# Performance work log

Measured on AMD Instinct MI355X. Metric: run time of the kernel, lower is better.

## Reference

```python
import jax, jax.numpy as jnp
import numpy as np

B, S, H, L, V, T = 128, 512, 512, 2, 30, 64  # batch, enc len, hidden, layers, vocab, decode len


def _p(k, shape):
    return jax.random.normal(k, shape, jnp.float32) * 0.05


def setup_inputs() -> dict:
    key = jax.random.key(0)
    ks = jax.random.split(key, 24)
    inp = {"x": jax.random.normal(ks[0], (B, S, 2), jnp.float32)}
    inp["emb"] = _p(ks[1], (V, H))
    # encoder GRU (input dim 2 for layer 0, H for layer 1); PyTorch gate order r,z,n
    inp["enc_Wih0"] = _p(ks[2], (3 * H, 2));  inp["enc_Whh0"] = _p(ks[3], (3 * H, H))
    inp["enc_bih0"] = _p(ks[4], (3 * H,));    inp["enc_bhh0"] = _p(ks[5], (3 * H,))
    inp["enc_Wih1"] = _p(ks[6], (3 * H, H));  inp["enc_Whh1"] = _p(ks[7], (3 * H, H))
    inp["enc_bih1"] = _p(ks[8], (3 * H,));    inp["enc_bhh1"] = _p(ks[9], (3 * H,))
    # decoder GRU (input dim H)
    inp["dec_Wih0"] = _p(ks[10], (3 * H, H)); inp["dec_Whh0"] = _p(ks[11], (3 * H, H))
    inp["dec_bih0"] = _p(ks[12], (3 * H,));   inp["dec_bhh0"] = _p(ks[13], (3 * H,))
    inp["dec_Wih1"] = _p(ks[14], (3 * H, H)); inp["dec_Whh1"] = _p(ks[15], (3 * H, H))
    inp["dec_bih1"] = _p(ks[16], (3 * H,));   inp["dec_bhh1"] = _p(ks[17], (3 * H,))
    inp["fc_W"] = _p(ks[18], (V, 2 * H));     inp["fc_b"] = _p(ks[19], (V,))
    return inp


def gru_cell(xt, h, Wih, Whh, bih, bhh):
    gi = xt @ Wih.T + bih
    gh = h @ Whh.T + bhh
    i_r, i_z, i_n = jnp.split(gi, 3, axis=-1)
    h_r, h_z, h_n = jnp.split(gh, 3, axis=-1)
    r = jax.nn.sigmoid(i_r + h_r)
    z = jax.nn.sigmoid(i_z + h_z)
    n = jnp.tanh(i_n + r * h_n)
    return (1.0 - z) * n + z * h


def _forward(x, emb,
             enc_Wih0, enc_Whh0, enc_bih0, enc_bhh0,
             enc_Wih1, enc_Whh1, enc_bih1, enc_bhh1,
             dec_Wih0, dec_Whh0, dec_bih0, dec_bhh0,
             dec_Wih1, dec_Whh1, dec_bih1, dec_bhh1,
             fc_W, fc_b):
    b = x.shape[0]
    h0 = jnp.zeros((b, H), x.dtype)

    # ---- encoder: 2-layer GRU scanned over time ----
    def enc_step(hs, xt):
        a = gru_cell(xt, hs[0], enc_Wih0, enc_Whh0, enc_bih0, enc_bhh0)
        c = gru_cell(a, hs[1], enc_Wih1, enc_Whh1, enc_bih1, enc_bhh1)
        return (a, c), c

    (e0, e1), out_enc_t = jax.lax.scan(enc_step, (h0, h0), x.transpose(1, 0, 2))
    out_enc = out_enc_t.transpose(1, 0, 2)  # [B, S, H]

    def dec_step(carry, _):
        (d0, d1), tok = carry
        e = emb[tok]  # [B, H]
        n0 = gru_cell(e, d0, dec_Wih0, dec_Whh0, dec_bih0, dec_bhh0)
        n1 = gru_cell(n0, d1, dec_Wih1, dec_Whh1, dec_bih1, dec_bhh1)
        out_dec = n1  # [B, H]
        sim = jnp.einsum('bsh,bh->bs', out_enc, out_dec)  # [B, S]
        # faithful to nn.Softmax() implicit dim on 3-D [B,S,1] tensor -> dim=0 (batch)
        att_w = jax.nn.softmax(sim, axis=0)
        attention = jnp.einsum('bs,bsh->bh', att_w, out_enc)  # [B, H]
        logits = jnp.concatenate([out_dec, attention], axis=-1) @ fc_W.T + fc_b  # [B, V]
        tok_next = jnp.argmax(logits, axis=-1)
        return ((n0, n1), tok_next), logits

    tok0 = jnp.zeros((b,), jnp.int32)
    ((f0, f1), _), logits_t = jax.lax.scan(dec_step, ((e0, e1), tok0), None, length=T)
    vec_out = logits_t.transpose(1, 0, 2)  # [B, T, V]
    hidden = jnp.stack([f0, f1], axis=0)   # [n_layers, B, H]
    return vec_out, hidden


def reference(x, emb,
              enc_Wih0, enc_Whh0, enc_bih0, enc_bhh0,
              enc_Wih1, enc_Whh1, enc_bih1, enc_bhh1,
              dec_Wih0, dec_Whh0, dec_bih0, dec_bhh0,
              dec_Wih1, dec_Whh1, dec_bih1, dec_bhh1,
              fc_W, fc_b):
    return _forward(x, emb,
                    enc_Wih0, enc_Whh0, enc_bih0, enc_bhh0,
                    enc_Wih1, enc_Whh1, enc_bih1, enc_bhh1,
                    dec_Wih0, dec_Whh0, dec_bih0, dec_bhh0,
                    dec_Wih1, dec_Whh1, dec_bih1, dec_bhh1,
                    fc_W, fc_b)
```

## Files before the change

### kernel.cpp

```cpp
#include <hip/hip_runtime.h>
#include <math.h>

typedef short  s16x8 __attribute__((ext_vector_type(8)));
typedef float  f32x4 __attribute__((ext_vector_type(4)));
typedef unsigned short u16;
typedef unsigned long long u64;

#define MFMA16(a, b, c) __builtin_amdgcn_mfma_f32_16x16x32_bf16((a), (b), (c), 0, 0, 0)

#define BB 128
#define SS 512
#define HH 512
#define VV 30
#define TT 64

#define SC_SYS  __HIP_MEMORY_SCOPE_SYSTEM

__device__ __forceinline__ float b2f(u16 v) {
  union { unsigned int u; float f; } c; c.u = ((unsigned int)v) << 16; return c.f;
}
__device__ __forceinline__ u16 f2b(float f) {
  union { float f; unsigned int u; } c; c.f = f;
  unsigned int r = (c.u + 0x7FFFu + ((c.u >> 16) & 1u)) >> 16;
  return (u16)r;
}
__device__ __forceinline__ float sigm(float x) { return 1.f / (1.f + expf(-x)); }
__device__ __forceinline__ s16x8 ldf(const u16* p) { return *(const s16x8*)p; }

__device__ __forceinline__ u64  ld64c(const u64* p)      { return __hip_atomic_load(p, __ATOMIC_RELAXED, SC_SYS); }
__device__ __forceinline__ void st64c(u64* p, u64 v)     { __hip_atomic_store(p, v, __ATOMIC_RELAXED, SC_SYS); }
__device__ __forceinline__ void stf32c(float* p, float v){ __hip_atomic_store(p, v, __ATOMIC_RELAXED, SC_SYS); }
__device__ __forceinline__ float ldf32c(const float* p)  { return __hip_atomic_load(p, __ATOMIC_RELAXED, SC_SYS); }
__device__ __forceinline__ void sti32c(int* p, int v)    { __hip_atomic_store(p, v, __ATOMIC_RELAXED, SC_SYS); }
__device__ __forceinline__ int  ldi32c(const int* p)     { return __hip_atomic_load(p, __ATOMIC_RELAXED, SC_SYS); }
__device__ __forceinline__ void stf32(float* p, float v) { *p = v; }

__device__ unsigned int g_cnt[128];
__device__ float g_smx[SS], g_ssum[SS];

#define C_L0 0
#define C_L1 1
#define C_G0 2
#define C_G1 3
#define C_SIM 4
#define C_SMX 5
#define C_ATT 6

__device__ __forceinline__ void waitp(int idx, int target) {
  if (target <= 0) return;
  unsigned long long t0 = __builtin_amdgcn_s_memrealtime();
  while ((int)__hip_atomic_load(&g_cnt[idx * 16], __ATOMIC_RELAXED, SC_SYS) < target) {
    __builtin_amdgcn_s_sleep(1);
    if (__builtin_amdgcn_s_memrealtime() - t0 > (1ull << 21)) break;
  }
}
__device__ __forceinline__ void waitc2(int i1, int t1, int i2, int t2) {
  if (threadIdx.x == 0) { waitp(i1, t1); waitp(i2, t2); }
  __syncthreads();
}
__device__ __forceinline__ void waitc3(int i1, int t1, int i2, int t2, int i3, int t3) {
  if (threadIdx.x == 0) { waitp(i1, t1); waitp(i2, t2); waitp(i3, t3); }
  __syncthreads();
}
__device__ __forceinline__ void waitc4(int i1, int t1, int i2, int t2, int i3, int t3, int i4, int t4) {
  if (threadIdx.x == 0) { waitp(i1, t1); waitp(i2, t2); waitp(i3, t3); waitp(i4, t4); }
  __syncthreads();
}
__device__ __forceinline__ void arrive(int idx) {
  __syncthreads();
  if (threadIdx.x == 0) {
    asm volatile("s_waitcnt vmcnt(0) lgkmcnt(0)" ::: "memory");
    __hip_atomic_fetch_add(&g_cnt[idx * 16], 1u, __ATOMIC_RELAXED, SC_SYS);
  }
}

__device__ __forceinline__ s16x8 ldl(const u16* buf, int row, int slot) {
  return *(const s16x8*)&buf[(row << 8) + ((slot ^ (row & 15)) << 3)];
}

__device__ __forceinline__ void stage64(u16* SMb, const u16* SRC, int mbase, int kc) {
  const int t = threadIdx.x;
  const u64* base = (const u64*)SRC;
  u64 v[16];
#pragma unroll
  for (int j = 0; j < 16; ++j) {
    const int g = kc * 8 + (j >> 1);
    const int half = j & 1;
    v[j] = ld64c(base + (size_t)(g * 128 + mbase + half * 32) * 8 + t);
  }
#pragma unroll
  for (int j = 0; j < 16; ++j) {
    const int gl = j >> 1, half = j & 1;
    const int row = half * 32 + (t >> 3);
    const int w = t & 7;
    const int s = ((w & 4) << 2) + 2 * gl + ((w >> 1) & 1);
    *(u64*)&SMb[(row << 8) + ((s ^ (row & 15)) << 3) + ((w & 1) << 2)] = v[j];
  }
}

__device__ __forceinline__ void stage128(u16* SM, const u16* SRC, int kc) {
  const int t = threadIdx.x;
  const u64* base = (const u64*)SRC;
  u64 v[32];
#pragma unroll
  for (int j = 0; j < 32; ++j) {
    const int g = kc * 8 + (j >> 2);
    const int q = j & 3;
    v[j] = ld64c(base + (size_t)(g * 128 + q * 32) * 8 + t);
  }
#pragma unroll
  for (int j = 0; j < 32; ++j) {
    const int gl = j >> 2, q = j & 3;
    const int row = q * 32 + (t >> 3);
    const int w = t & 7;
    const int s = ((w & 4) << 2) + 2 * gl + ((w >> 1) & 1);
    *(u64*)&SM[(row << 8) + ((s ^ (row & 15)) << 3) + ((w & 1) << 2)] = v[j];
  }
}


template <bool GATHER, bool COH_H>
__device__ __forceinline__ void gru_dual_staged(
    int bx, u16* SM,
    const u16* __restrict__ A1s, const int* __restrict__ gather,
    const u16* __restrict__ A2s,
    const u16* __restrict__ Wihs, const u16* __restrict__ Whhs,
    const float* __restrict__ bih, const float* __restrict__ bhh,
    float* __restrict__ hf, u16* __restrict__ hs_new,
    u16* __restrict__ oe, size_t oe_mstride)
{
  const int tid  = threadIdx.x;
  const int wave = tid >> 6, lane = tid & 63;
  const int lrow = lane & 15, lq = lane >> 4;
  const int gidx = bx >> 1;
  const int j0 = gidx * 16;
  const int mbase = (bx & 1) * 64;
  const int lr = wave * 16 + lrow;
  const int m0 = mbase + wave * 16;

  const u16* a1p = nullptr;
  if (GATHER)
    a1p = A1s + (size_t)ldi32c(&gather[m0 + lrow]) * 1024 + lq * 8;

  const u16* bp[6];
#pragma unroll
  for (int t = 0; t < 6; ++t) {
    int g = (t < 3) ? t : t - 3;
    const u16* W = (t < 3) ? Wihs : Whhs;
    bp[t] = W + (size_t)(g * HH + j0 + lrow) * 1024 + lq * 8;
  }

  f32x4 acc[6];
#pragma unroll
  for (int t = 0; t < 6; ++t) acc[t] = (f32x4){0.f, 0.f, 0.f, 0.f};

  for (int kc = 0; kc < 4; ++kc) {
    if (!GATHER) stage64(SM, A1s, mbase, kc);
    stage64(SM + 64 * 256, A2s, mbase, kc);
    __syncthreads();
#pragma unroll
    for (int ki = 0; ki < 4; ++ki) {
      const int sl = ki * 4 + lq;
      s16x8 a1h, a1l;
      if (GATHER) { a1h = ldf(a1p); a1l = ldf(a1p + 512); a1p += 32; }
      else        { a1h = ldl(SM, lr, sl); a1l = ldl(SM, lr, 16 + sl); }
      s16x8 a2h = ldl(SM, 64 + lr, sl), a2l = ldl(SM, 64 + lr, 16 + sl);
#pragma unroll
      for (int t = 0; t < 6; ++t) {
        s16x8 bh = ldf(bp[t]), bl = ldf(bp[t] + 512); bp[t] += 32;
        s16x8 ah = (t < 3) ? a1h : a2h;
        s16x8 al = (t < 3) ? a1l : a2l;
        acc[t] = MFMA16(ah, bh, acc[t]);
        acc[t] = MFMA16(ah, bl, acc[t]);
        acc[t] = MFMA16(al, bh, acc[t]);
      }
    }
    __syncthreads();
  }

  const int c = j0 + lrow;
  const float bir = bih[c], biz = bih[HH + c], bin = bih[2 * HH + c];
  const float bhr = bhh[c], bhz = bhh[HH + c], bhn = bhh[2 * HH + c];
  float hvv[4];
#pragma unroll
  for (int r = 0; r < 4; ++r) {
    int m = mbase + wave * 16 + lq * 4 + r;
    float ir = acc[0][r] + bir, iz = acc[1][r] + biz, inn = acc[2][r] + bin;
    float hr = acc[3][r] + bhr, hz = acc[4][r] + bhz, hn = acc[5][r] + bhn;
    float rr = sigm(ir + hr);
    float zz = sigm(iz + hz);
    float nn = tanhf(inn + rr * hn);
    float hp = COH_H ? ldf32c(&hf[(size_t)m * HH + c]) : hf[(size_t)m * HH + c];
    float hv = (1.f - zz) * nn + zz * hp;
    if (COH_H) stf32c(&hf[(size_t)m * HH + c], hv);
    else       stf32(&hf[(size_t)m * HH + c], hv);
    hvv[r] = hv;
    if (oe) oe[(size_t)m * oe_mstride + c] = f2b(hv);
  }
  __syncthreads();
#pragma unroll
  for (int r = 0; r < 4; ++r) {
    const int ml = wave * 16 + lq * 4 + r;
    u16 hi = f2b(hvv[r]);
    SM[ml * 32 + lrow]      = hi;
    SM[ml * 32 + 16 + lrow] = f2b(hvv[r] - b2f(hi));
  }
  __syncthreads();
  {
    u64* dst = (u64*)hs_new + (size_t)(gidx * 128 + mbase) * 8;
    const u64* src = (const u64*)SM;
    st64c(dst + tid,       src[tid]);
    st64c(dst + 256 + tid, src[256 + tid]);
  }
}

__device__ __forceinline__ void gru_l0_staged(
    int bx, int p, u16* SM,
    const float* __restrict__ x, const float* __restrict__ Wih0,
    const u16* __restrict__ Whh0s,
    const float* __restrict__ bih0, const float* __restrict__ bhh0,
    const u16* __restrict__ As,
    float* __restrict__ af, u16* __restrict__ as_new)
{
  const int tid  = threadIdx.x;
  const int wave = tid >> 6, lane = tid & 63;
  const int lrow = lane & 15, lq = lane >> 4;
  const int j0 = bx * 16;
  const int mw = wave * 32;
  const int r0 = mw + lrow, r1 = mw + 16 + lrow;

  const u16* bp[3];
#pragma unroll
  for (int t = 0; t < 3; ++t)
    bp[t] = Whh0s + (size_t)(t * HH + j0 + lrow) * 1024 + lq * 8;

  f32x4 acc[2][3];
#pragma unroll
  for (int i = 0; i < 2; ++i)
#pragma unroll
    for (int t = 0; t < 3; ++t) acc[i][t] = (f32x4){0.f, 0.f, 0.f, 0.f};

  for (int kc = 0; kc < 4; ++kc) {
    stage128(SM, As, kc);
    __syncthreads();
#pragma unroll
    for (int ki = 0; ki < 4; ++ki) {
      const int sl = ki * 4 + lq;
      s16x8 a0h = ldl(SM, r0, sl), a0l = ldl(SM, r0, 16 + sl);
      s16x8 a1h = ldl(SM, r1, sl), a1l = ldl(SM, r1, 16 + sl);
#pragma unroll
      for (int t = 0; t < 3; ++t) {
        s16x8 bh = ldf(bp[t]), bl = ldf(bp[t] + 512); bp[t] += 32;
        acc[0][t] = MFMA16(a0h, bh, acc[0][t]);
        acc[0][t] = MFMA16(a0h, bl, acc[0][t]);
        acc[0][t] = MFMA16(a0l, bh, acc[0][t]);
        acc[1][t] = MFMA16(a1h, bh, acc[1][t]);
        acc[1][t] = MFMA16(a1h, bl, acc[1][t]);
        acc[1][t] = MFMA16(a1l, bh, acc[1][t]);
      }
    }
    __syncthreads();
  }

  const int c = j0 + lrow;
  const float bir = bih0[c], biz = bih0[HH + c], bin = bih0[2 * HH + c];
  const float bhr = bhh0[c], bhz = bhh0[HH + c], bhn = bhh0[2 * HH + c];
  const float wr0 = Wih0[(size_t)c * 2],            wr1 = Wih0[(size_t)c * 2 + 1];
  const float wz0 = Wih0[(size_t)(HH + c) * 2],     wz1 = Wih0[(size_t)(HH + c) * 2 + 1];
  const float wn0 = Wih0[(size_t)(2 * HH + c) * 2], wn1 = Wih0[(size_t)(2 * HH + c) * 2 + 1];
  float hvv[2][4];
#pragma unroll
  for (int tm = 0; tm < 2; ++tm) {
#pragma unroll
    for (int r = 0; r < 4; ++r) {
      int m = mw + tm * 16 + lq * 4 + r;
      float x0 = x[((size_t)m * SS + p) * 2];
      float x1 = x[((size_t)m * SS + p) * 2 + 1];
      float ir  = bir + x0 * wr0 + x1 * wr1;
      float iz  = biz + x0 * wz0 + x1 * wz1;
      float inn = bin + x0 * wn0 + x1 * wn1;
      float hr = acc[tm][0][r] + bhr, hz = acc[tm][1][r] + bhz, hn = acc[tm][2][r] + bhn;
      float rr = sigm(ir + hr);
      float zz = sigm(iz + hz);
      float nn = tanhf(inn + rr * hn);
      float hp = af[(size_t)m * HH + c];
      float hv = (1.f - zz) * nn + zz * hp;
      af[(size_t)m * HH + c] = hv;
      hvv[tm][r] = hv;
    }
  }
  __syncthreads();
#pragma unroll
  for (int tm = 0; tm < 2; ++tm) {
#pragma unroll
    for (int r = 0; r < 4; ++r) {
      const int ml = mw + tm * 16 + lq * 4 + r;
      u16 hi = f2b(hvv[tm][r]);
      SM[ml * 32 + lrow]      = hi;
      SM[ml * 32 + 16 + lrow] = f2b(hvv[tm][r] - b2f(hi));
    }
  }
  __syncthreads();
  {
    u64* dst = (u64*)as_new + (size_t)(bx * 128) * 8;
    const u64* src = (const u64*)SM;
#pragma unroll
    for (int k = 0; k < 4; ++k)
      st64c(dst + k * 256 + tid, src[k * 256 + tid]);
  }
}

__device__ __forceinline__ void sim_block(
    int bx, const float* __restrict__ n1f, const u16* __restrict__ oe,
    float* __restrict__ simt)
{
  const int b = bx >> 1, sc = bx & 1;
  const int wave = threadIdx.x >> 6, lane = threadIdx.x & 63;
  float xr[8];
  const u64* xp = (const u64*)(n1f + (size_t)b * HH + lane * 8);
#pragma unroll
  for (int j = 0; j < 4; ++j) {
    union { u64 q; float f[2]; } u; u.q = ld64c(xp + j);
    xr[2 * j] = u.f[0]; xr[2 * j + 1] = u.f[1];
  }
  int s0 = sc * 256 + wave * 64;
  for (int i = 0; i < 64; ++i) {
    int s = s0 + i;
    s16x8 ov = *(const s16x8*)(oe + ((size_t)b * SS + s) * HH + lane * 8);
    float acc = 0.f;
#pragma unroll
    for (int j = 0; j < 8; ++j) acc += xr[j] * b2f((u16)ov[j]);
    for (int off = 32; off; off >>= 1) acc += __shfl_down(acc, off);
    if (lane == 0) stf32c(&simt[(size_t)s * BB + b], acc);
  }
}

__device__ __forceinline__ void smax_block(int bx, const float* __restrict__ simt)
{
  const int wave = threadIdx.x >> 6, lane = threadIdx.x & 63;
  const int s = bx * 4 + wave;
  union { u64 q; float f[2]; } u;
  u.q = ld64c((const u64*)&simt[(size_t)s * BB + lane * 2]);
  float mx = fmaxf(u.f[0], u.f[1]);
  for (int off = 32; off; off >>= 1) mx = fmaxf(mx, __shfl_xor(mx, off));
  float e = expf(u.f[0] - mx) + expf(u.f[1] - mx);
  for (int off = 32; off; off >>= 1) e += __shfl_xor(e, off);
  if (lane == 0) { stf32c(&g_smx[s], mx); stf32c(&g_ssum[s], e); }
}

__device__ __forceinline__ void attn_block(
    int b, int tstep, const float* __restrict__ simt, const float* __restrict__ n1f,
    const u16* __restrict__ oe, const float* __restrict__ fcW,
    const float* __restrict__ fcb, float* __restrict__ dout,
    int* __restrict__ tok)
{
  __shared__ float wsm[SS];
  __shared__ float xv[2 * HH];
  __shared__ float lg[32];
  const int t = threadIdx.x;

  for (int s = t; s < SS; s += 256) {
    float sv = ldf32c(&simt[(size_t)s * BB + b]);
    float mx = ldf32c(&g_smx[s]);
    float sm = ldf32c(&g_ssum[s]);
    wsm[s] = expf(sv - mx) / sm;
  }
  xv[t]       = ldf32c(&n1f[(size_t)b * HH + t]);
  xv[t + 256] = ldf32c(&n1f[(size_t)b * HH + t + 256]);
  __syncthreads();

  {
    float a0 = 0.f, a1 = 0.f;
    const u16* base = oe + (size_t)b * SS * HH;
    for (int s = 0; s < SS; ++s) {
      float w = wsm[s];
      a0 += w * b2f(base[(size_t)s * HH + t]);
      a1 += w * b2f(base[(size_t)s * HH + t + 256]);
    }
    xv[HH + t]       = a0;
    xv[HH + t + 256] = a1;
  }
  __syncthreads();

  int wave = t >> 6, lane = t & 63;
  for (int v = wave; v < VV; v += 4) {
    const float* wr = fcW + (size_t)v * (2 * HH);
    float acc = 0.f;
#pragma unroll
    for (int i = 0; i < 16; ++i) acc += xv[i * 64 + lane] * wr[i * 64 + lane];
    for (int off = 32; off; off >>= 1) acc += __shfl_down(acc, off);
    if (lane == 0) {
      float lv = acc + fcb[v];
      lg[v] = lv;
      dout[(size_t)b * (TT * VV) + (size_t)tstep * VV + v] = lv;
    }
  }
  __syncthreads();

  if (t == 0) {
    float best = lg[0]; int bi = 0;
    for (int v = 1; v < VV; ++v) if (lg[v] > best) { best = lg[v]; bi = v; }
    sti32c(&tok[b], bi);
  }
}

__global__ __launch_bounds__(256) void enc_persist(
    const float* __restrict__ x, const float* __restrict__ Wih0,
    const u16* __restrict__ Whh0s,
    const float* __restrict__ bih0, const float* __restrict__ bhh0,
    const u16* __restrict__ Wih1s, const u16* __restrict__ Whh1s,
    const float* __restrict__ bih1, const float* __restrict__ bhh1,
    u16* ABF0, u16* ABF1, float* af,
    u16* CBF0, u16* CBF1, float* cf,
    u16* out_enc)
{
  __shared__ u16 SM[32768];
  const int bx = blockIdx.x;
  const u16* pa = ABF0; u16* pa_n = ABF1;
  const u16* pc = CBF0; u16* pc_n = CBF1;
  for (int p = 0; p <= SS; ++p) {
    waitc2(C_L0, 32 * p, C_L1, 64 * (p - 1));
    if (bx < 32) {
      if (p < SS) {
        gru_l0_staged(bx, p, SM, x, Wih0, Whh0s, bih0, bhh0, pa, af, pa_n);
        arrive(C_L0);
      }
    } else {
      if (p > 0) {
        u16* oe = out_enc + (size_t)(p - 1) * HH;
        gru_dual_staged<false, false>(bx - 32, SM, pa, nullptr, pc,
                                      Wih1s, Whh1s, bih1, bhh1,
                                      cf, pc_n, oe, (size_t)SS * HH);
        arrive(C_L1);
      }
    }
    const u16* tp;
    tp = pa; pa = pa_n; pa_n = (u16*)tp;
    tp = pc; pc = pc_n; pc_n = (u16*)tp;
  }
}

__global__ __launch_bounds__(256) void dec_persist(
    const u16* __restrict__ EMBs, int* tok,
    const u16* __restrict__ WdIH0, const u16* __restrict__ WdHH0,
    const float* __restrict__ dbih0, const float* __restrict__ dbhh0,
    const u16* __restrict__ WdIH1, const u16* __restrict__ WdHH1,
    const float* __restrict__ dbih1, const float* __restrict__ dbhh1,
    float* af, float* cf,
    u16* D0A, u16* D0B, u16* D1A, u16* D1B,
    const u16* __restrict__ oe, float* simt,
    const float* __restrict__ fcW, const float* __restrict__ fcb,
    float* dout)
{
  __shared__ u16 SM[32768];
  const int bx = blockIdx.x;
  const u16* d0c = D0A; u16* d0n = D0B;
  const u16* d1c = D1A; u16* d1n = D1B;
  for (int t = 0; t < TT; ++t) {
    if (bx < 64) {
      waitc3(C_G0, 64 * t, C_ATT, 128 * t, C_G1, 64 * (t - 1));
      gru_dual_staged<true, false>(bx, SM, EMBs, tok, d0c,
                                   WdIH0, WdHH0, dbih0, dbhh0, af, d0n,
                                   nullptr, 0);
      arrive(C_G0);
    }
    { const u16* tp = d0c; d0c = d0n; d0n = (u16*)tp; }

    if (bx < 64) {
      waitc4(C_G0, 64 * (t + 1), C_G1, 64 * t, C_SIM, 256 * t, C_ATT, 128 * t);
      gru_dual_staged<false, true>(bx, SM, d0c, nullptr, d1c,
                                   WdIH1, WdHH1, dbih1, dbhh1, cf, d1n,
                                   nullptr, 0);
      arrive(C_G1);
    }
    { const u16* tp = d1c; d1c = d1n; d1n = (u16*)tp; }

    waitc3(C_G1, 64 * (t + 1), C_SMX, 128 * t, C_ATT, 128 * t);
    sim_block(bx, cf, oe, simt);
    arrive(C_SIM);

    if (bx < 128) {
      waitc2(C_SIM, 256 * (t + 1), C_ATT, 128 * t);
      smax_block(bx, simt);
      arrive(C_SMX);
    }

    if (bx < BB) {
      waitc4(C_SMX, 128 * (t + 1), C_SIM, 256 * (t + 1),
             C_G1, 64 * (t + 1), C_G0, 64 * (t + 1));
      attn_block(bx, t, simt, cf, oe, fcW, fcb, dout, tok);
      arrive(C_ATT);
    }
  }
}

__global__ __launch_bounds__(256) void splitall(
    const float* __restrict__ s0, u16* d0, const float* __restrict__ s1, u16* d1,
    const float* __restrict__ s2, u16* d2, const float* __restrict__ s3, u16* d3,
    const float* __restrict__ s4, u16* d4, const float* __restrict__ s5, u16* d5,
    const float* __restrict__ s6, u16* d6, const float* __restrict__ s7, u16* d7)
{
  const int WN = 3 * HH * HH;
  int i = blockIdx.x * 256 + threadIdx.x;
  const float* s; u16* d; int j;
  if      (i < 1 * WN) { s = s0; d = d0; j = i; }
  else if (i < 2 * WN) { s = s1; d = d1; j = i - 1 * WN; }
  else if (i < 3 * WN) { s = s2; d = d2; j = i - 2 * WN; }
  else if (i < 4 * WN) { s = s3; d = d3; j = i - 3 * WN; }
  else if (i < 5 * WN) { s = s4; d = d4; j = i - 4 * WN; }
  else if (i < 6 * WN) { s = s5; d = d5; j = i - 5 * WN; }
  else if (i < 7 * WN) { s = s6; d = d6; j = i - 6 * WN; }
  else { j = i - 7 * WN; if (j >= VV * HH) return; s = s7; d = d7; }
  int r = j >> 9, k = j & 511;
  float v = s[j];
  u16 hi = f2b(v);
  d[(size_t)r * 1024 + k]       = hi;
  d[(size_t)r * 1024 + 512 + k] = f2b(v - b2f(hi));
}

__global__ __launch_bounds__(256) void initk(
    float* af, float* cf, u16* b0, u16* b1, u16* b2, u16* b3, int* tok)
{
  int i = blockIdx.x * 256 + threadIdx.x;
  b0[i] = 0; b1[i] = 0; b2[i] = 0; b3[i] = 0;
  if (i < BB * HH) { af[i] = 0.f; cf[i] = 0.f; }
  if (i < BB) tok[i] = 0;
  if (i < 128) g_cnt[i] = 0;
}

__global__ __launch_bounds__(256) void finalize(
    const float* __restrict__ d0, const float* __restrict__ d1,
    float* __restrict__ oh)
{
  int i = blockIdx.x * 256 + threadIdx.x;
  oh[i]           = d0[i];
  oh[BB * HH + i] = d1[i];
}

extern "C" void kernel_launch(void* const* d_in, const int* in_sizes, int n_in,
                              void* d_out, int out_size, void* d_ws, size_t ws_size,
                              hipStream_t stream) {
  const float* x     = (const float*)d_in[0];
  const float* emb   = (const float*)d_in[1];
  const float* eWih0 = (const float*)d_in[2];
  const float* eWhh0 = (const float*)d_in[3];
  const float* ebih0 = (const float*)d_in[4];
  const float* ebhh0 = (const float*)d_in[5];
  const float* eWih1 = (const float*)d_in[6];
  const float* eWhh1 = (const float*)d_in[7];
  const float* ebih1 = (const float*)d_in[8];
  const float* ebhh1 = (const float*)d_in[9];
  const float* dWih0 = (const float*)d_in[10];
  const float* dWhh0 = (const float*)d_in[11];
  const float* dbih0 = (const float*)d_in[12];
  const float* dbhh0 = (const float*)d_in[13];
  const float* dWih1 = (const float*)d_in[14];
  const float* dWhh1 = (const float*)d_in[15];
  const float* dbih1 = (const float*)d_in[16];
  const float* dbhh1 = (const float*)d_in[17];
  const float* fcW   = (const float*)d_in[18];
  const float* fcb   = (const float*)d_in[19];
  float* dout = (float*)d_out;

  char* wsb = (char*)d_ws;
  float* af   = (float*)(wsb + 0);
  float* cf   = (float*)(wsb + 262144);
  u16* ABF0   = (u16*)(wsb + 524288);
  u16* ABF1   = (u16*)(wsb + 786432);
  u16* CBF0   = (u16*)(wsb + 1048576);
  u16* CBF1   = (u16*)(wsb + 1310720);
  int* tok    = (int*)(wsb + 1572864);
  float* simt = (float*)(wsb + 1573376);
  u16* WeHH0  = (u16*)(wsb + 1835520);
  u16* WeIH1  = (u16*)(wsb + 4981248);
  u16* WeHH1  = (u16*)(wsb + 8126976);
  u16* WdIH0  = (u16*)(wsb + 11272704);
  u16* WdHH0  = (u16*)(wsb + 14418432);
  u16* WdIH1  = (u16*)(wsb + 17564160);
  u16* WdHH1  = (u16*)(wsb + 20709888);
  u16* EMBs   = (u16*)(wsb + 23855616);
  u16* oe     = (u16*)(wsb + 23917056);

  initk<<<512, 256, 0, stream>>>(af, cf, ABF0, ABF1, CBF0, CBF1, tok);

  splitall<<<21564, 256, 0, stream>>>(eWhh0, WeHH0, eWih1, WeIH1, eWhh1, WeHH1,
                                      dWih0, WdIH0, dWhh0, WdHH0, dWih1, WdIH1,
                                      dWhh1, WdHH1, emb, EMBs);

  enc_persist<<<96, 256, 0, stream>>>(x, eWih0, WeHH0, ebih0, ebhh0,
                                      WeIH1, WeHH1, ebih1, ebhh1,
                                      ABF0, ABF1, af, CBF0, CBF1, cf, oe);

  dec_persist<<<256, 256, 0, stream>>>(EMBs, tok, WdIH0, WdHH0, dbih0, dbhh0,
                                       WdIH1, WdHH1, dbih1, dbhh1,
                                       af, cf, ABF0, ABF1, CBF1, CBF0,
                                       oe, simt, fcW, fcb, dout);

  finalize<<<256, 256, 0, stream>>>(af, cf, dout + (size_t)BB * TT * VV);
}
```

Baseline: 25.54 ms.

## Replace atomic counter barriers with per-block flag slots polled in parallel

Swaps the shared atomic fetch-add counters used for cross-block synchronisation in the persistent encoder and decoder kernels for one flag slot per producer block. Each producer stores its step number with a plain store, and consumers poll many slots at once across threads rather than having thread 0 spin on several counters. This removes atomic contention on a few hot cache lines and trims some redundant waits. The cost is more polling traffic per wait, and correctness now rests on transitive ordering through the remaining dependencies.

```diff
diff --git a/kernel.cpp b/kernel.cpp
--- a/kernel.cpp
+++ b/kernel.cpp
@@ -35,43 +35,40 @@
 __device__ __forceinline__ int  ldi32c(const int* p)     { return __hip_atomic_load(p, __ATOMIC_RELAXED, SC_SYS); }
 __device__ __forceinline__ void stf32(float* p, float v) { *p = v; }
 
-__device__ unsigned int g_cnt[128];
+__device__ unsigned int g_slot[736 * 16];
 __device__ float g_smx[SS], g_ssum[SS];
 
-#define C_L0 0
-#define C_L1 1
-#define C_G0 2
-#define C_G1 3
-#define C_SIM 4
-#define C_SMX 5
-#define C_ATT 6
-
-__device__ __forceinline__ void waitp(int idx, int target) {
+#define S_L0  0
+#define S_L1  32
+#define S_G0  96
+#define S_G1  160
+#define S_SIM 224
+#define S_SMX 480
+#define S_ATT 608
+
+__device__ __forceinline__ void pollslot(int idx, int target) {
   if (target <= 0) return;
+  const unsigned int* p = &g_slot[idx * 16];
   unsigned long long t0 = __builtin_amdgcn_s_memrealtime();
-  while ((int)__hip_atomic_load(&g_cnt[idx * 16], __ATOMIC_RELAXED, SC_SYS) < target) {
+  while ((int)__hip_atomic_load(p, __ATOMIC_RELAXED, SC_SYS) < target) {
     __builtin_amdgcn_s_sleep(1);
     if (__builtin_amdgcn_s_memrealtime() - t0 > (1ull << 21)) break;
   }
 }
-__device__ __forceinline__ void waitc2(int i1, int t1, int i2, int t2) {
-  if (threadIdx.x == 0) { waitp(i1, t1); waitp(i2, t2); }
-  __syncthreads();
-}
-__device__ __forceinline__ void waitc3(int i1, int t1, int i2, int t2, int i3, int t3) {
-  if (threadIdx.x == 0) { waitp(i1, t1); waitp(i2, t2); waitp(i3, t3); }
-  __syncthreads();
-}
-__device__ __forceinline__ void waitc4(int i1, int t1, int i2, int t2, int i3, int t3, int i4, int t4) {
-  if (threadIdx.x == 0) { waitp(i1, t1); waitp(i2, t2); waitp(i3, t3); waitp(i4, t4); }
-  __syncthreads();
-}
-__device__ __forceinline__ void arrive(int idx) {
-  __syncthreads();
-  if (threadIdx.x == 0) {
-    asm volatile("s_waitcnt vmcnt(0) lgkmcnt(0)" ::: "memory");
-    __hip_atomic_fetch_add(&g_cnt[idx * 16], 1u, __ATOMIC_RELAXED, SC_SYS);
-  }
+__device__ __forceinline__ void wait_group(int base, int n, int target) {
+  if ((int)threadIdx.x < n) pollslot(base + (int)threadIdx.x, target);
+  __syncthreads();
+}
+__device__ __forceinline__ void enc_wait(int p) {
+  const int t = threadIdx.x;
+  if (t < 32) pollslot(S_L0 + t, p);
+  else if (t < 96) pollslot(S_L1 + (t - 32), p - 1);
+  __syncthreads();
+}
+__device__ __forceinline__ void postslot(int idx, int val) {
+  __syncthreads();
+  if (threadIdx.x == 0)
+    __hip_atomic_store(&g_slot[idx * 16], (unsigned int)val, __ATOMIC_RELAXED, SC_SYS);
 }
 
 __device__ __forceinline__ s16x8 ldl(const u16* buf, int row, int slot) {
@@ -419,11 +416,11 @@
   const u16* pa = ABF0; u16* pa_n = ABF1;
   const u16* pc = CBF0; u16* pc_n = CBF1;
   for (int p = 0; p <= SS; ++p) {
-    waitc2(C_L0, 32 * p, C_L1, 64 * (p - 1));
+    enc_wait(p);
     if (bx < 32) {
       if (p < SS) {
         gru_l0_staged(bx, p, SM, x, Wih0, Whh0s, bih0, bhh0, pa, af, pa_n);
-        arrive(C_L0);
+        postslot(S_L0 + bx, p + 1);
       }
     } else {
       if (p > 0) {
@@ -431,7 +428,7 @@
         gru_dual_staged<false, false>(bx - 32, SM, pa, nullptr, pc,
                                       Wih1s, Whh1s, bih1, bhh1,
                                       cf, pc_n, oe, (size_t)SS * HH);
-        arrive(C_L1);
+        postslot(S_L1 + (bx - 32), p);
       }
     }
     const u16* tp;
@@ -458,38 +455,37 @@
   const u16* d1c = D1A; u16* d1n = D1B;
   for (int t = 0; t < TT; ++t) {
     if (bx < 64) {
-      waitc3(C_G0, 64 * t, C_ATT, 128 * t, C_G1, 64 * (t - 1));
+      wait_group(S_ATT, 128, t);
       gru_dual_staged<true, false>(bx, SM, EMBs, tok, d0c,
                                    WdIH0, WdHH0, dbih0, dbhh0, af, d0n,
                                    nullptr, 0);
-      arrive(C_G0);
+      postslot(S_G0 + bx, t + 1);
     }
     { const u16* tp = d0c; d0c = d0n; d0n = (u16*)tp; }
 
     if (bx < 64) {
-      waitc4(C_G0, 64 * (t + 1), C_G1, 64 * t, C_SIM, 256 * t, C_ATT, 128 * t);
+      wait_group(S_G0, 64, t + 1);
       gru_dual_staged<false, true>(bx, SM, d0c, nullptr, d1c,
                                    WdIH1, WdHH1, dbih1, dbhh1, cf, d1n,
                                    nullptr, 0);
-      arrive(C_G1);
+      postslot(S_G1 + bx, t + 1);
     }
     { const u16* tp = d1c; d1c = d1n; d1n = (u16*)tp; }
 
-    waitc3(C_G1, 64 * (t + 1), C_SMX, 128 * t, C_ATT, 128 * t);
+    wait_group(S_G1, 64, t + 1);
     sim_block(bx, cf, oe, simt);
-    arrive(C_SIM);
+    postslot(S_SIM + bx, t + 1);
 
     if (bx < 128) {
-      waitc2(C_SIM, 256 * (t + 1), C_ATT, 128 * t);
+      wait_group(S_SIM, 256, t + 1);
       smax_block(bx, simt);
-      arrive(C_SMX);
+      postslot(S_SMX + bx, t + 1);
     }
 
     if (bx < BB) {
-      waitc4(C_SMX, 128 * (t + 1), C_SIM, 256 * (t + 1),
-             C_G1, 64 * (t + 1), C_G0, 64 * (t + 1));
+      wait_group(S_SMX, 128, t + 1);
       attn_block(bx, t, simt, cf, oe, fcW, fcb, dout, tok);
-      arrive(C_ATT);
+      postslot(S_ATT + bx, t + 1);
     }
   }
 }
@@ -525,7 +521,7 @@
   b0[i] = 0; b1[i] = 0; b2[i] = 0; b3[i] = 0;
   if (i < BB * HH) { af[i] = 0.f; cf[i] = 0.f; }
   if (i < BB) tok[i] = 0;
-  if (i < 128) g_cnt[i] = 0;
+  if (i < 736) g_slot[i * 16] = 0;
 }
 
 __global__ __launch_bounds__(256) void finalize(
```

Measured after the change: 24.02 ms, median of 2. -6.0%, faster.
